# Kernel optimization log

Measured on AMD Instinct MI355X. Metric: run time of the kernel, lower is better.

## Reference

```python
import jax, jax.numpy as jnp
import numpy as np

N = 50000
E = 800000
IN_DIM, HID_DIM, OUT_DIM = 128, 64, 32


def setup_inputs() -> dict:
    key = jax.random.key(0)
    k1, k2, k3, k4 = jax.random.split(key, 4)
    x = jax.random.normal(k1, (N, IN_DIM), dtype=jnp.float32)
    edge_index = jax.random.randint(k2, (2, E), 0, N, dtype=jnp.int64)
    # Glorot-style init for GCNConv weights, zero bias (PyG default)
    W1 = jax.random.normal(k3, (IN_DIM, HID_DIM), dtype=jnp.float32) / np.sqrt(IN_DIM)
    b1 = jnp.zeros((HID_DIM,), dtype=jnp.float32)
    W2 = jax.random.normal(k4, (HID_DIM, OUT_DIM), dtype=jnp.float32) / np.sqrt(HID_DIM)
    b2 = jnp.zeros((OUT_DIM,), dtype=jnp.float32)
    return {"x": x, "edge_index": edge_index, "W1": W1, "b1": b1, "W2": W2, "b2": b2}


def _gcn_norm(edge_index, num_nodes):
    # Add self-loops (PyG GCNConv default add_self_loops=True)
    loops = jnp.arange(num_nodes, dtype=edge_index.dtype)
    row = jnp.concatenate([edge_index[0], loops])  # source
    col = jnp.concatenate([edge_index[1], loops])  # target
    deg = jax.ops.segment_sum(jnp.ones_like(col, dtype=jnp.float32), col,
                              num_segments=num_nodes)
    dis = jnp.where(deg > 0, jax.lax.rsqrt(jnp.maximum(deg, 1.0)), 0.0)
    norm = dis[row] * dis[col]  # [E+N]
    return row, col, norm


def _gcn_conv(h, row, col, norm, W, b, num_nodes):
    h = h @ W                                   # [N, out]
    msg = h[row] * norm[:, None]                # gather + scale, [E+N, out]
    out = jax.ops.segment_sum(msg, col, num_segments=num_nodes)
    return out + b


def reference(x, edge_index, W1, b1, W2, b2):
    num_nodes = x.shape[0]
    row, col, norm = _gcn_norm(edge_index, num_nodes)
    h = _gcn_conv(x, row, col, norm, W1, b1, num_nodes)
    h = jax.nn.relu(h)
    out = _gcn_conv(h, row, col, norm, W2, b2, num_nodes)
    return out
```

## Files before the change

kernel.cpp:

```cpp
#include <hip/hip_runtime.h>
#include <hip/hip_fp16.h>

#define Nn    50000
#define Ee    800000
#define IND   128
#define HIDD  64
#define OUTD  32
#define NBUCK ((Nn + 255) / 256)
#define EPB   4096
#define NBB   ((Ee + EPB - 1) / EPB)
#define SCAP  6144
#define RB    64
#define GB    ((Nn + RB - 1) / RB)

__device__ __forceinline__ int ld_nt_i32(const int* p) {
    return __builtin_nontemporal_load(p);
}
__device__ __forceinline__ long long ld_nt_i64(const long long* p) {
    return __builtin_nontemporal_load(p);
}

__global__ __launch_bounds__(256) void k_bin(const void* __restrict__ p,
        int* __restrict__ gcur, unsigned int* __restrict__ staged) {
    __shared__ int hist[256], offs[256], lcur[256], gposs[256];
    __shared__ unsigned int stage[EPB];
    __shared__ unsigned int red[256];
    int t = threadIdx.x;
    int base0 = blockIdx.x * EPB;
    red[t] = ((const unsigned int*)p)[2 * (base0 + t) + 1];
    hist[t] = 0;
    __syncthreads();
    for (int s = 128; s > 0; s >>= 1) {
        if (t < s) red[t] |= red[t + s];
        __syncthreads();
    }
    bool f64 = (red[0] == 0u);
    int nv = Ee - base0; if (nv > EPB) nv = EPB;
    unsigned int pl[16];
    #pragma unroll
    for (int q = 0; q < 16; ++q) {
        int e = base0 + q * 256 + t;
        if (e < Ee) {
            int r, c;
            if (f64) { r = (int)ld_nt_i64((const long long*)p + e);
                       c = (int)ld_nt_i64((const long long*)p + Ee + e); }
            else     { r = ld_nt_i32((const int*)p + e);
                       c = ld_nt_i32((const int*)p + Ee + e); }
            pl[q] = ((unsigned int)c << 16) | (unsigned int)r;
            atomicAdd(&hist[pl[q] >> 24], 1);
        }
    }
    __syncthreads();
    int v = hist[t];
    offs[t] = v;
    __syncthreads();
    for (int off = 1; off < 256; off <<= 1) {
        int add = (t >= off) ? offs[t - off] : 0;
        __syncthreads();
        offs[t] += add;
        __syncthreads();
    }
    int excl = offs[t] - v;
    __syncthreads();
    offs[t] = excl;
    lcur[t] = excl;
    __syncthreads();
    #pragma unroll
    for (int q = 0; q < 16; ++q) {
        int e = base0 + q * 256 + t;
        if (e < Ee) {
            int bk = pl[q] >> 24;
            int pos = atomicAdd(&lcur[bk], 1);
            stage[pos] = pl[q];
        }
    }
    if (t < NBUCK) {
        int h = hist[t];
        gposs[t] = h ? atomicAdd(&gcur[t], h) : 0;
    }
    __syncthreads();
    for (int i = t; i < nv; i += 256) {
        unsigned int pv = stage[i];
        int bk = pv >> 24;
        int idx = gposs[bk] + (i - offs[bk]);
        if (idx < SCAP) staged[(size_t)bk * SCAP + idx] = pv;
    }
}

__global__ __launch_bounds__(256) void k_bsort(const unsigned int* __restrict__ staged,
        const int* __restrict__ gcur, int* __restrict__ rowstart,
        float* __restrict__ dis, unsigned short* __restrict__ slots) {
    __shared__ int bsc[256];
    __shared__ int hist[256], nodestart[256], cur[256];
    __shared__ unsigned short sortbuf[SCAP];
    int t = threadIdx.x, b = blockIdx.x;
    int gv = (t < NBUCK) ? min(gcur[t], SCAP) : 0;
    bsc[t] = gv;
    hist[t] = 0;
    __syncthreads();
    for (int off = 1; off < 256; off <<= 1) {
        int add = (t >= off) ? bsc[t - off] : 0;
        __syncthreads();
        bsc[t] += add;
        __syncthreads();
    }
    int bucketbase = (b == 0) ? 0 : bsc[b - 1];
    int m = bsc[b] - bucketbase;
    const unsigned int* sp = staged + (size_t)b * SCAP;
    for (int i = t; i < m; i += 256) atomicAdd(&hist[(sp[i] >> 16) & 255], 1);
    __syncthreads();
    int v = hist[t];
    nodestart[t] = v;
    __syncthreads();
    for (int off = 1; off < 256; off <<= 1) {
        int add = (t >= off) ? nodestart[t - off] : 0;
        __syncthreads();
        nodestart[t] += add;
        __syncthreads();
    }
    int excl = nodestart[t] - v;
    __syncthreads();
    nodestart[t] = excl;
    cur[t] = 0;
    int node = b * 256 + t;
    if (node < Nn) {
        rowstart[node] = bucketbase + excl;
        dis[node] = rsqrtf((float)v + 1.0f);
    }
    if (b == NBUCK - 1 && t == 0) rowstart[Nn] = Ee;
    __syncthreads();
    for (int i = t; i < m; i += 256) {
        unsigned int pv = sp[i];
        int lc = (pv >> 16) & 255;
        int pos = nodestart[lc] + atomicAdd(&cur[lc], 1);
        sortbuf[pos] = (unsigned short)(pv & 0xFFFFu);
    }
    __syncthreads();
    for (int i = t; i < m; i += 256) slots[bucketbase + i] = sortbuf[i];
}

__global__ __launch_bounds__(256) void k_gemm1(const float* __restrict__ x,
                                               const float* __restrict__ W,
                                               const float* __restrict__ dis,
                                               __half* __restrict__ h) {
    __shared__ float xs[RB][IND + 4];
    __shared__ float Ws[IND * HIDD];
    int t = threadIdx.x;
    int row0 = blockIdx.x * RB;
    for (int i = t; i < IND * HIDD / 4; i += 256)
        ((float4*)Ws)[i] = ((const float4*)W)[i];
    for (int i = t; i < RB * IND / 4; i += 256) {
        int rr = i >> 5, cc = (i & 31) * 4;
        int gr = row0 + rr;
        float4 v = make_float4(0.f, 0.f, 0.f, 0.f);
        if (gr < Nn) v = ((const float4*)x)[(size_t)gr * (IND / 4) + (i & 31)];
        *(float4*)&xs[rr][cc] = v;
    }
    __syncthreads();
    int jg = t & 15, rg = t >> 4;
    float acc[4][4] = {{0.f,0.f,0.f,0.f},{0.f,0.f,0.f,0.f},
                       {0.f,0.f,0.f,0.f},{0.f,0.f,0.f,0.f}};
    for (int k = 0; k < IND; k += 4) {
        float4 xv0 = *(const float4*)&xs[rg * 4 + 0][k];
        float4 xv1 = *(const float4*)&xs[rg * 4 + 1][k];
        float4 xv2 = *(const float4*)&xs[rg * 4 + 2][k];
        float4 xv3 = *(const float4*)&xs[rg * 4 + 3][k];
        float4 w0 = *(const float4*)&Ws[(k + 0) * HIDD + jg * 4];
        float4 w1 = *(const float4*)&Ws[(k + 1) * HIDD + jg * 4];
        float4 w2 = *(const float4*)&Ws[(k + 2) * HIDD + jg * 4];
        float4 w3 = *(const float4*)&Ws[(k + 3) * HIDD + jg * 4];
        #define ROWSTEP(XV, R) \
            acc[R][0]=fmaf(XV.x,w0.x,acc[R][0]); acc[R][1]=fmaf(XV.x,w0.y,acc[R][1]); \
            acc[R][2]=fmaf(XV.x,w0.z,acc[R][2]); acc[R][3]=fmaf(XV.x,w0.w,acc[R][3]); \
            acc[R][0]=fmaf(XV.y,w1.x,acc[R][0]); acc[R][1]=fmaf(XV.y,w1.y,acc[R][1]); \
            acc[R][2]=fmaf(XV.y,w1.z,acc[R][2]); acc[R][3]=fmaf(XV.y,w1.w,acc[R][3]); \
            acc[R][0]=fmaf(XV.z,w2.x,acc[R][0]); acc[R][1]=fmaf(XV.z,w2.y,acc[R][1]); \
            acc[R][2]=fmaf(XV.z,w2.z,acc[R][2]); acc[R][3]=fmaf(XV.z,w2.w,acc[R][3]); \
            acc[R][0]=fmaf(XV.w,w3.x,acc[R][0]); acc[R][1]=fmaf(XV.w,w3.y,acc[R][1]); \
            acc[R][2]=fmaf(XV.w,w3.z,acc[R][2]); acc[R][3]=fmaf(XV.w,w3.w,acc[R][3]);
        ROWSTEP(xv0, 0) ROWSTEP(xv1, 1) ROWSTEP(xv2, 2) ROWSTEP(xv3, 3)
        #undef ROWSTEP
    }
    #pragma unroll
    for (int rr = 0; rr < 4; ++rr) {
        int gr = row0 + rg * 4 + rr;
        if (gr < Nn) {
            float d = dis[gr];
            __half2 lo = __floats2half2_rn(d * acc[rr][0], d * acc[rr][1]);
            __half2 hi = __floats2half2_rn(d * acc[rr][2], d * acc[rr][3]);
            uint2 pk = make_uint2(*(unsigned int*)&lo, *(unsigned int*)&hi);
            *(uint2*)&h[(size_t)gr * HIDD + jg * 4] = pk;
        }
    }
}

__global__ __launch_bounds__(256) void k_agg1(const unsigned short* __restrict__ slots,
        const int* __restrict__ rowstart, const float* __restrict__ dis,
        const __half2* __restrict__ h1, const float* __restrict__ b1,
        const float* __restrict__ W2, __half* __restrict__ h2) {
    __shared__ float sh[8][HIDD];
    __shared__ float W2s[HIDD * OUTD];
    int t = threadIdx.x;
    for (int i = t; i < HIDD * OUTD; i += 256) W2s[i] = W2[i];
    int sub = t >> 5, lane = t & 31;
    int n = blockIdx.x * 8 + sub;
    int s = rowstart[n], e = rowstart[n + 1];
    float d = dis[n];
    float2 acc = make_float2(0.f, 0.f);
    int p = s;
    for (; p + 8 <= e; p += 8) {
        int rv[8];
        #pragma unroll
        for (int q = 0; q < 8; ++q) rv[q] = slots[p + q];
        float2 fv[8];
        #pragma unroll
        for (int q = 0; q < 8; ++q) fv[q] = __half22float2(h1[rv[q] * 32 + lane]);
        #pragma unroll
        for (int q = 0; q < 8; ++q) { acc.x += fv[q].x; acc.y += fv[q].y; }
    }
    for (; p < e; ++p) {
        float2 v = __half22float2(h1[(int)slots[p] * 32 + lane]);
        acc.x += v.x; acc.y += v.y;
    }
    float2 self = __half22float2(h1[n * 32 + lane]);
    float vx = b1[2 * lane]     + d * (acc.x + self.x);
    float vy = b1[2 * lane + 1] + d * (acc.y + self.y);
    sh[sub][2 * lane]     = fmaxf(vx, 0.0f);
    sh[sub][2 * lane + 1] = fmaxf(vy, 0.0f);
    __syncthreads();
    int jn = t >> 5, j = t & 31;
    float o = 0.0f;
    #pragma unroll
    for (int k = 0; k < HIDD; ++k) o = fmaf(sh[jn][k], W2s[k * OUTD + j], o);
    h2[(size_t)n * OUTD + j] = __float2half(d * o);
}

__global__ __launch_bounds__(256) void k_agg2(const unsigned short* __restrict__ slots,
        const int* __restrict__ rowstart, const float* __restrict__ dis,
        const __half2* __restrict__ h2, const float* __restrict__ b2,
        float* __restrict__ out) {
    int t = threadIdx.x;
    int sub = t >> 4, lane = t & 15;
    int n = blockIdx.x * 16 + sub;
    int s = rowstart[n], e = rowstart[n + 1];
    float d = dis[n];
    float2 acc = make_float2(0.f, 0.f);
    int p = s;
    for (; p + 8 <= e; p += 8) {
        int rv[8];
        #pragma unroll
        for (int q = 0; q < 8; ++q) rv[q] = slots[p + q];
        float2 fv[8];
        #pragma unroll
        for (int q = 0; q < 8; ++q) fv[q] = __half22float2(h2[rv[q] * 16 + lane]);
        #pragma unroll
        for (int q = 0; q < 8; ++q) { acc.x += fv[q].x; acc.y += fv[q].y; }
    }
    for (; p < e; ++p) {
        float2 v = __half22float2(h2[(int)slots[p] * 16 + lane]);
        acc.x += v.x; acc.y += v.y;
    }
    float2 self = __half22float2(h2[n * 16 + lane]);
    float2 res;
    res.x = b2[2 * lane]     + d * (acc.x + self.x);
    res.y = b2[2 * lane + 1] + d * (acc.y + self.y);
    ((float2*)out)[n * 16 + lane] = res;
}

extern "C" void kernel_launch(void* const* d_in, const int* in_sizes, int n_in,
                              void* d_out, int out_size, void* d_ws, size_t ws_size,
                              hipStream_t stream) {
    const float* x  = (const float*)d_in[0];
    const void*  ei = d_in[1];
    const float* W1 = (const float*)d_in[2];
    const float* b1 = (const float*)d_in[3];
    const float* W2 = (const float*)d_in[4];
    const float* b2 = (const float*)d_in[5];
    float* out = (float*)d_out;

    char* w = (char*)d_ws;
    int*            gcur     = (int*)w;            w += ((size_t)NBUCK * 4 + 255) / 256 * 256;
    int*            rowstart = (int*)w;            w += (size_t)(Nn + 1) * 4 + 188;
    float*          dis      = (float*)w;          w += (size_t)Nn * 4;
    unsigned int*   staged   = (unsigned int*)w;   w += (size_t)NBUCK * SCAP * 4;
    unsigned short* slots    = (unsigned short*)w; w += (size_t)Ee * 2;
    __half*         h1       = (__half*)w;         w += (size_t)Nn * HIDD * 2;
    __half*         h2       = (__half*)w;         w += (size_t)Nn * OUTD * 2;

    hipMemsetAsync(gcur, 0, (size_t)NBUCK * 4, stream);
    k_bin  <<<NBB, 256, 0, stream>>>(ei, gcur, staged);
    k_bsort<<<NBUCK, 256, 0, stream>>>(staged, gcur, rowstart, dis, slots);
    k_gemm1<<<GB, 256, 0, stream>>>(x, W1, dis, h1);
    k_agg1 <<<Nn / 8, 256, 0, stream>>>(slots, rowstart, dis, (const __half2*)h1, b1, W2, h2);
    k_agg2 <<<Nn / 16, 256, 0, stream>>>(slots, rowstart, dis, (const __half2*)h2, b2, out);
}
```

Before: 178.9 us.

## Use fp16 MFMA for first GEMM and deepen gather unrolling in aggregations

The first dense projection now converts x and a transposed W1 to fp16 in shared memory and computes it with 16x16x32 MFMA instructions instead of scalar fp32 FMAs. Both aggregation kernels now issue 16 neighbour gathers per iteration before falling back to 8 and then 1, to keep more memory loads in flight. The MFMA path rounds inputs to fp16, which adds precision loss. Its output stores become scalar half writes rather than packed 8-byte writes, and the deeper unroll raises register pressure.

```diff
diff --git a/kernel.cpp b/kernel.cpp
--- a/kernel.cpp
+++ b/kernel.cpp
@@ -12,6 +12,10 @@
 #define SCAP  6144
 #define RB    64
 #define GB    ((Nn + RB - 1) / RB)
+#define XSTR  136
+
+typedef _Float16 f16x8 __attribute__((ext_vector_type(8)));
+typedef float    f32x4 __attribute__((ext_vector_type(4)));
 
 __device__ __forceinline__ int ld_nt_i32(const int* p) {
     return __builtin_nontemporal_load(p);
@@ -143,53 +147,47 @@
                                                const float* __restrict__ W,
                                                const float* __restrict__ dis,
                                                __half* __restrict__ h) {
-    __shared__ float xs[RB][IND + 4];
-    __shared__ float Ws[IND * HIDD];
+    __shared__ _Float16 Xl[RB * XSTR];
+    __shared__ _Float16 Wl[HIDD * XSTR];
     int t = threadIdx.x;
     int row0 = blockIdx.x * RB;
-    for (int i = t; i < IND * HIDD / 4; i += 256)
-        ((float4*)Ws)[i] = ((const float4*)W)[i];
-    for (int i = t; i < RB * IND / 4; i += 256) {
-        int rr = i >> 5, cc = (i & 31) * 4;
+    for (int i = t; i < IND * HIDD; i += 256) {
+        int k = i & 127, n = i >> 7;
+        Wl[n * XSTR + k] = (_Float16)W[k * HIDD + n];
+    }
+    for (int i = t; i < RB * (IND / 4); i += 256) {
+        int rr = i >> 5, kk = (i & 31) * 4;
         int gr = row0 + rr;
         float4 v = make_float4(0.f, 0.f, 0.f, 0.f);
         if (gr < Nn) v = ((const float4*)x)[(size_t)gr * (IND / 4) + (i & 31)];
-        *(float4*)&xs[rr][cc] = v;
-    }
-    __syncthreads();
-    int jg = t & 15, rg = t >> 4;
-    float acc[4][4] = {{0.f,0.f,0.f,0.f},{0.f,0.f,0.f,0.f},
-                       {0.f,0.f,0.f,0.f},{0.f,0.f,0.f,0.f}};
-    for (int k = 0; k < IND; k += 4) {
-        float4 xv0 = *(const float4*)&xs[rg * 4 + 0][k];
-        float4 xv1 = *(const float4*)&xs[rg * 4 + 1][k];
-        float4 xv2 = *(const float4*)&xs[rg * 4 + 2][k];
-        float4 xv3 = *(const float4*)&xs[rg * 4 + 3][k];
-        float4 w0 = *(const float4*)&Ws[(k + 0) * HIDD + jg * 4];
-        float4 w1 = *(const float4*)&Ws[(k + 1) * HIDD + jg * 4];
-        float4 w2 = *(const float4*)&Ws[(k + 2) * HIDD + jg * 4];
-        float4 w3 = *(const float4*)&Ws[(k + 3) * HIDD + jg * 4];
-        #define ROWSTEP(XV, R) \
-            acc[R][0]=fmaf(XV.x,w0.x,acc[R][0]); acc[R][1]=fmaf(XV.x,w0.y,acc[R][1]); \
-            acc[R][2]=fmaf(XV.x,w0.z,acc[R][2]); acc[R][3]=fmaf(XV.x,w0.w,acc[R][3]); \
-            acc[R][0]=fmaf(XV.y,w1.x,acc[R][0]); acc[R][1]=fmaf(XV.y,w1.y,acc[R][1]); \
-            acc[R][2]=fmaf(XV.y,w1.z,acc[R][2]); acc[R][3]=fmaf(XV.y,w1.w,acc[R][3]); \
-            acc[R][0]=fmaf(XV.z,w2.x,acc[R][0]); acc[R][1]=fmaf(XV.z,w2.y,acc[R][1]); \
-            acc[R][2]=fmaf(XV.z,w2.z,acc[R][2]); acc[R][3]=fmaf(XV.z,w2.w,acc[R][3]); \
-            acc[R][0]=fmaf(XV.w,w3.x,acc[R][0]); acc[R][1]=fmaf(XV.w,w3.y,acc[R][1]); \
-            acc[R][2]=fmaf(XV.w,w3.z,acc[R][2]); acc[R][3]=fmaf(XV.w,w3.w,acc[R][3]);
-        ROWSTEP(xv0, 0) ROWSTEP(xv1, 1) ROWSTEP(xv2, 2) ROWSTEP(xv3, 3)
-        #undef ROWSTEP
-    }
-    #pragma unroll
-    for (int rr = 0; rr < 4; ++rr) {
-        int gr = row0 + rg * 4 + rr;
+        _Float16* dst = &Xl[rr * XSTR + kk];
+        dst[0] = (_Float16)v.x; dst[1] = (_Float16)v.y;
+        dst[2] = (_Float16)v.z; dst[3] = (_Float16)v.w;
+    }
+    __syncthreads();
+    int wv = t >> 6, lane = t & 63;
+    int m = lane & 15, quad = lane >> 4;
+    f32x4 acc[4] = {{0.f,0.f,0.f,0.f},{0.f,0.f,0.f,0.f},
+                    {0.f,0.f,0.f,0.f},{0.f,0.f,0.f,0.f}};
+    const _Float16* xrow = &Xl[(wv * 16 + m) * XSTR + quad * 8];
+    #pragma unroll
+    for (int kt = 0; kt < 4; ++kt) {
+        f16x8 av = *(const f16x8*)(xrow + kt * 32);
+        #pragma unroll
+        for (int ct = 0; ct < 4; ++ct) {
+            f16x8 bv = *(const f16x8*)&Wl[(ct * 16 + m) * XSTR + kt * 32 + quad * 8];
+            acc[ct] = __builtin_amdgcn_mfma_f32_16x16x32_f16(av, bv, acc[ct], 0, 0, 0);
+        }
+    }
+    int rbase = row0 + wv * 16 + quad * 4;
+    #pragma unroll
+    for (int reg = 0; reg < 4; ++reg) {
+        int gr = rbase + reg;
         if (gr < Nn) {
             float d = dis[gr];
-            __half2 lo = __floats2half2_rn(d * acc[rr][0], d * acc[rr][1]);
-            __half2 hi = __floats2half2_rn(d * acc[rr][2], d * acc[rr][3]);
-            uint2 pk = make_uint2(*(unsigned int*)&lo, *(unsigned int*)&hi);
-            *(uint2*)&h[(size_t)gr * HIDD + jg * 4] = pk;
+            #pragma unroll
+            for (int ct = 0; ct < 4; ++ct)
+                h[(size_t)gr * HIDD + ct * 16 + m] = __float2half(d * acc[ct][reg]);
         }
     }
 }
@@ -208,7 +206,18 @@
     float d = dis[n];
     float2 acc = make_float2(0.f, 0.f);
     int p = s;
-    for (; p + 8 <= e; p += 8) {
+    while (p + 16 <= e) {
+        int rv[16];
+        #pragma unroll
+        for (int q = 0; q < 16; ++q) rv[q] = slots[p + q];
+        float2 fv[16];
+        #pragma unroll
+        for (int q = 0; q < 16; ++q) fv[q] = __half22float2(h1[rv[q] * 32 + lane]);
+        #pragma unroll
+        for (int q = 0; q < 16; ++q) { acc.x += fv[q].x; acc.y += fv[q].y; }
+        p += 16;
+    }
+    if (p + 8 <= e) {
         int rv[8];
         #pragma unroll
         for (int q = 0; q < 8; ++q) rv[q] = slots[p + q];
@@ -217,6 +226,7 @@
         for (int q = 0; q < 8; ++q) fv[q] = __half22float2(h1[rv[q] * 32 + lane]);
         #pragma unroll
         for (int q = 0; q < 8; ++q) { acc.x += fv[q].x; acc.y += fv[q].y; }
+        p += 8;
     }
     for (; p < e; ++p) {
         float2 v = __half22float2(h1[(int)slots[p] * 32 + lane]);
@@ -246,7 +256,18 @@
     float d = dis[n];
     float2 acc = make_float2(0.f, 0.f);
     int p = s;
-    for (; p + 8 <= e; p += 8) {
+    while (p + 16 <= e) {
+        int rv[16];
+        #pragma unroll
+        for (int q = 0; q < 16; ++q) rv[q] = slots[p + q];
+        float2 fv[16];
+        #pragma unroll
+        for (int q = 0; q < 16; ++q) fv[q] = __half22float2(h2[rv[q] * 16 + lane]);
+        #pragma unroll
+        for (int q = 0; q < 16; ++q) { acc.x += fv[q].x; acc.y += fv[q].y; }
+        p += 16;
+    }
+    if (p + 8 <= e) {
         int rv[8];
         #pragma unroll
         for (int q = 0; q < 8; ++q) rv[q] = slots[p + q];
@@ -255,6 +276,7 @@
         for (int q = 0; q < 8; ++q) fv[q] = __half22float2(h2[rv[q] * 16 + lane]);
         #pragma unroll
         for (int q = 0; q < 8; ++q) { acc.x += fv[q].x; acc.y += fv[q].y; }
+        p += 8;
     }
     for (; p < e; ++p) {
         float2 v = __half22float2(h2[(int)slots[p] * 16 + lane]);
```

Measured after the change: 177.7 us. About the same (-0.6%).
